# Performance work log

Hardware: AMD Instinct MI355X
Metric: run time of the kernel (lower is better)

Reference implementation:

```python
import jax, jax.numpy as jnp
import numpy as np

BATCH, SEQ, D_IN, D_STATE = 8, 4096, 1024, 64


def setup_inputs() -> dict:
    key = jax.random.key(0)
    ks = jax.random.split(key, 3)
    u = jax.random.normal(ks[0], (BATCH, SEQ, D_IN), dtype=jnp.float32)
    log_A = jnp.zeros((D_STATE,), dtype=jnp.float32)
    B = jax.random.normal(ks[1], (D_STATE, D_IN), dtype=jnp.float32) * 0.01
    C = jax.random.normal(ks[2], (D_IN, D_STATE), dtype=jnp.float32) * 0.01
    D = jnp.ones((D_IN,), dtype=jnp.float32)
    log_delta = jnp.zeros((D_IN,), dtype=jnp.float32)
    return {"u": u, "log_A": log_A, "B": B, "C": C, "D": D, "log_delta": log_delta}


def reference(u, log_A, B, C, D, log_delta):
    batch, seq_len, input_dim = u.shape
    state_dim = log_A.shape[0]
    delta = jax.nn.softplus(log_delta)                      # [I]
    A = -jnp.exp(log_A)                                     # [N]
    A_bar = jnp.exp(delta[:, None] * A[None, :])            # [I, N]
    A_bar_state = A_bar.mean(axis=0)                        # [N]
    B_bar = B * delta[None, :]                              # [N, I]
    # Precompute input projections for all timesteps: [B, T, N]
    Bu = jnp.einsum('ni,bti->btn', B_bar, u)
    x0 = jnp.zeros((batch, state_dim), dtype=u.dtype)

    def step(x, bu_t):
        x = x * A_bar_state[None, :] + bu_t
        return x, x

    _, xs = jax.lax.scan(step, x0, jnp.swapaxes(Bu, 0, 1))  # xs: [T, B, N]
    xs = jnp.swapaxes(xs, 0, 1)                             # [B, T, N]
    y = jnp.einsum('in,btn->bti', C, xs) + D[None, None, :] * u
    return y
```

## Files before the change

kernel.cpp:

```cpp
#include <hip/hip_runtime.h>
#include <hip/hip_bf16.h>
#include <cstdint>

#define BATCH 8
#define SEQ   4096
#define DIN   1024
#define DST   64
#define CHUNK 64
#define NC    (SEQ/CHUNK)

typedef __attribute__((ext_vector_type(8))) short short8;
typedef __attribute__((ext_vector_type(4))) short short4v;
typedef __attribute__((ext_vector_type(4))) float f32x4;

__device__ __forceinline__ short f2bf(float f) {
    union { float f; unsigned u; } v; v.f = f;
    unsigned r = v.u + 0x7fffu + ((v.u >> 16) & 1u);
    return (short)(r >> 16);
}
__device__ __forceinline__ float softplus_f(float x) {
    return (x > 20.f) ? x : log1pf(expf(x));
}

__global__ void ssm_k0(const float* __restrict__ logA, const float* __restrict__ Bm,
                       const float* __restrict__ Cm, const float* __restrict__ logdelta,
                       short* __restrict__ Bb, short* __restrict__ Cb,
                       float* __restrict__ a_o, float* __restrict__ l2a_o,
                       float* __restrict__ aL_o)
{
    __shared__ float red[256];
    int blk = blockIdx.x, tid = threadIdx.x;
    if (blk < DST) {
        int n = blk;
        float An = -expf(logA[n]);
        float acc = 0.f;
        #pragma unroll
        for (int ii = 0; ii < DIN/256; ++ii) {
            int i = ii*256 + tid;
            float dlt = softplus_f(logdelta[i]);
            Bb[n*DIN + i] = f2bf(Bm[n*DIN + i] * dlt);
            acc += expf(dlt * An);
        }
        red[tid] = acc; __syncthreads();
        for (int s = 128; s > 0; s >>= 1) {
            if (tid < s) red[tid] += red[tid + s];
            __syncthreads();
        }
        if (tid == 0) {
            float a = red[0] * (1.f/DIN);
            a_o[n]   = a;
            l2a_o[n] = log2f(a);
            float p = a;
            #pragma unroll
            for (int q = 0; q < 6; ++q) p = p*p;
            aL_o[n] = p;
        }
    } else {
        int base = (blk - DST) * (DIN*DST/16);
        for (int e = tid; e < DIN*DST/16; e += 256)
            Cb[base + e] = f2bf(Cm[base + e]);
    }
}

__global__ __launch_bounds__(512) void ssm_k1(
    const float* __restrict__ u, const short* __restrict__ Bb,
    const float* __restrict__ a_i, float* __restrict__ xloc, float* __restrict__ carry)
{
    int blk = blockIdx.x;
    int b = blk >> 6, c = blk & (NC-1);
    int tid = threadIdx.x;
    int w = tid >> 6, lane = tid & 63;
    int wr = w & 3, wk = w >> 2;
    int m = lane & 15, quad = lane >> 4;

    long row = ((long)b << 12) + (c << 6) + (wr << 4) + m;
    const float* up  = u  + row * DIN + wk*(DIN/2) + quad * 8;
    const short* bb0 = Bb + wk*(DIN/2) + quad * 8;

    f32x4 acc0 = {0,0,0,0}, acc1 = {0,0,0,0}, acc2 = {0,0,0,0}, acc3 = {0,0,0,0};

    #pragma unroll 4
    for (int ks = 0; ks < DIN/64; ++ks) {
        const float4* uv = (const float4*)(up + ks*32);
        float4 ua = uv[0];
        float4 ub = uv[1];
        short8 af;
        af[0]=f2bf(ua.x); af[1]=f2bf(ua.y); af[2]=f2bf(ua.z); af[3]=f2bf(ua.w);
        af[4]=f2bf(ub.x); af[5]=f2bf(ub.y); af[6]=f2bf(ub.z); af[7]=f2bf(ub.w);
        const short* bbase = bb0 + ks*32;
        short8 b0 = *(const short8*)(bbase + ( 0 + m)*DIN);
        short8 b1 = *(const short8*)(bbase + (16 + m)*DIN);
        short8 b2 = *(const short8*)(bbase + (32 + m)*DIN);
        short8 b3 = *(const short8*)(bbase + (48 + m)*DIN);
        acc0 = __builtin_amdgcn_mfma_f32_16x16x32_bf16(af, b0, acc0, 0,0,0);
        acc1 = __builtin_amdgcn_mfma_f32_16x16x32_bf16(af, b1, acc1, 0,0,0);
        acc2 = __builtin_amdgcn_mfma_f32_16x16x32_bf16(af, b2, acc2, 0,0,0);
        acc3 = __builtin_amdgcn_mfma_f32_16x16x32_bf16(af, b3, acc3, 0,0,0);
    }

    __shared__ float bu[2][CHUNK][DST];
    int trow = (wr << 4) + (quad << 2);
    #pragma unroll
    for (int r = 0; r < 4; ++r) {
        bu[wk][trow + r][ 0 + m] = acc0[r];
        bu[wk][trow + r][16 + m] = acc1[r];
        bu[wk][trow + r][32 + m] = acc2[r];
        bu[wk][trow + r][48 + m] = acc3[r];
    }
    __syncthreads();

    if (tid < DST) {
        int n = tid;
        float an = a_i[n];
        float x = 0.f;
        float* xp = xloc + (((long)b << 12) + (c << 6)) * DST + n;
        #pragma unroll 8
        for (int t = 0; t < CHUNK; ++t) {
            x = x * an + (bu[0][t][n] + bu[1][t][n]);
            xp[(long)t * DST] = x;
        }
        carry[(b * NC + c) * DST + n] = x;
    }
}

__global__ void ssm_k2(const float* __restrict__ carry, const float* __restrict__ aL,
                       float* __restrict__ Xin)
{
    int b = blockIdx.x, n = threadIdx.x;
    float cr[NC];
    #pragma unroll
    for (int c = 0; c < NC; ++c)
        cr[c] = carry[(b*NC + c)*DST + n];
    float x = 0.f, al = aL[n];
    #pragma unroll
    for (int c = 0; c < NC; ++c) {
        Xin[(b*NC + c)*DST + n] = x;
        x = x * al + cr[c];
    }
}

__global__ __launch_bounds__(256) void ssm_k3(
    const float* __restrict__ u, const float* __restrict__ xloc,
    const float* __restrict__ Xin, const float* __restrict__ l2a,
    const short* __restrict__ Cb, const float* __restrict__ Dv,
    float* __restrict__ y)
{
    int tblk = blockIdx.x;
    long t0 = (long)tblk << 4;
    int b = (int)(t0 >> 12);
    int tloc0 = (int)(t0 & (SEQ-1));
    int chunk = tloc0 >> 6;
    int jbase = tloc0 & (CHUNK-1);

    __shared__ short xb[16][DST];

    int tid = threadIdx.x;
    {
        int m  = tid >> 4;
        int n0 = (tid & 15) * 4;
        long t = t0 + m;
        int j  = jbase + m;
        float4 xv = *(const float4*)(xloc + t*DST + n0);
        float4 xi = *(const float4*)(Xin + (long)(b*NC + chunk)*DST + n0);
        float4 la = *(const float4*)(l2a + n0);
        float jp = (float)(j + 1);
        short4v xs;
        xs[0] = f2bf(xv.x + exp2f(jp*la.x)*xi.x);
        xs[1] = f2bf(xv.y + exp2f(jp*la.y)*xi.y);
        xs[2] = f2bf(xv.z + exp2f(jp*la.z)*xi.z);
        xs[3] = f2bf(xv.w + exp2f(jp*la.w)*xi.w);
        *(short4v*)(&xb[m][n0]) = xs;
    }
    __syncthreads();

    int w = tid >> 6, lane = tid & 63;
    int l16 = lane & 15, quad = lane >> 4;

    short8 x0 = *(const short8*)(&xb[l16][ 0 + quad*8]);
    short8 x1 = *(const short8*)(&xb[l16][32 + quad*8]);

    long trow = t0 + l16;
    const float* urow = u + trow*DIN;
    float* yrow = y + trow*DIN;

    #pragma unroll 4
    for (int ii = 0; ii < 16; ++ii) {
        int i0 = (ii*4 + w) * 16;
        const short* cb = Cb + (long)(i0 + l16)*DST + quad*8;
        short8 c0 = *(const short8*)(cb);
        short8 c1 = *(const short8*)(cb + 32);
        f32x4 acc = {0,0,0,0};
        acc = __builtin_amdgcn_mfma_f32_16x16x32_bf16(c0, x0, acc, 0,0,0);
        acc = __builtin_amdgcn_mfma_f32_16x16x32_bf16(c1, x1, acc, 0,0,0);
        int ib = i0 + (quad << 2);
        float4 dd = *(const float4*)(Dv + ib);
        float4 uu = *(const float4*)(urow + ib);
        float4 o;
        o.x = acc[0] + dd.x*uu.x;
        o.y = acc[1] + dd.y*uu.y;
        o.z = acc[2] + dd.z*uu.z;
        o.w = acc[3] + dd.w*uu.w;
        *(float4*)(yrow + ib) = o;
    }
}

extern "C" void kernel_launch(void* const* d_in, const int* in_sizes, int n_in,
                              void* d_out, int out_size, void* d_ws, size_t ws_size,
                              hipStream_t stream)
{
    const float* u        = (const float*)d_in[0];
    const float* logA     = (const float*)d_in[1];
    const float* Bm       = (const float*)d_in[2];
    const float* Cm       = (const float*)d_in[3];
    const float* D        = (const float*)d_in[4];
    const float* logdelta = (const float*)d_in[5];
    float* y = (float*)d_out;

    char* ws = (char*)d_ws;
    float* xloc  = (float*)(ws);
    float* carry = (float*)(ws + 8u*1024*1024);
    float* Xin   = (float*)(ws + 8u*1024*1024 + 128*1024);
    short* Bb    = (short*)(ws + 8u*1024*1024 + 256*1024);
    short* Cb    = (short*)(ws + 8u*1024*1024 + 384*1024);
    float* a_o   = (float*)(ws + 8u*1024*1024 + 512*1024);
    float* l2a_o = a_o + 64;
    float* aL_o  = a_o + 128;

    hipLaunchKernelGGL(ssm_k0, dim3(DST + 16), dim3(256), 0, stream,
                       logA, Bm, Cm, logdelta, Bb, Cb, a_o, l2a_o, aL_o);
    hipLaunchKernelGGL(ssm_k1, dim3(BATCH*NC), dim3(512), 0, stream,
                       u, Bb, a_o, xloc, carry);
    hipLaunchKernelGGL(ssm_k2, dim3(BATCH), dim3(DST), 0, stream,
                       carry, aL_o, Xin);
    hipLaunchKernelGGL(ssm_k3, dim3((BATCH*SEQ)/16), dim3(256), 0, stream,
                       u, xloc, Xin, l2a_o, Cb, D, y);
}
```

Before: 320.0 us.

## Fuse chunk scan, carry propagation and output projection into one kernel with decoupled lookback

Merges the per-chunk Bu GEMM and local scan, the cross-chunk carry scan, and the C projection plus D*u into a single kernel. Chunks are ordered by an atomic ticket, and each chunk gets its carry-in through a decoupled lookback over global flags. The local states stay in LDS, so the 8MB xloc buffer is never written and read back, and two kernel launches go away. The cost is serialized lookback spin waits, a second pass over u inside the same block, and only 512 blocks doing the output GEMM instead of 2048.

Measured after the change: 405.6 us. 26.7% more time.

```diff
diff --git a/kernel.cpp b/kernel.cpp
--- a/kernel.cpp
+++ b/kernel.cpp
@@ -1,5 +1,4 @@
 #include <hip/hip_runtime.h>
-#include <hip/hip_bf16.h>
 #include <cstdint>
 
 #define BATCH 8
@@ -8,9 +7,9 @@
 #define DST   64
 #define CHUNK 64
 #define NC    (SEQ/CHUNK)
+#define NBLK  (BATCH*NC)
 
 typedef __attribute__((ext_vector_type(8))) short short8;
-typedef __attribute__((ext_vector_type(4))) short short4v;
 typedef __attribute__((ext_vector_type(4))) float f32x4;
 
 __device__ __forceinline__ short f2bf(float f) {
@@ -26,7 +25,7 @@
                        const float* __restrict__ Cm, const float* __restrict__ logdelta,
                        short* __restrict__ Bb, short* __restrict__ Cb,
                        float* __restrict__ a_o, float* __restrict__ l2a_o,
-                       float* __restrict__ aL_o)
+                       float* __restrict__ aL_o, unsigned* __restrict__ ctl)
 {
     __shared__ float red[256];
     int blk = blockIdx.x, tid = threadIdx.x;
@@ -56,151 +55,156 @@
             aL_o[n] = p;
         }
     } else {
+        if (blk == DST) {
+            for (int g = tid; g <= NBLK; g += 256) ctl[g] = 0u;
+        }
         int base = (blk - DST) * (DIN*DST/16);
         for (int e = tid; e < DIN*DST/16; e += 256)
             Cb[base + e] = f2bf(Cm[base + e]);
     }
 }
 
-__global__ __launch_bounds__(512) void ssm_k1(
+__global__ __launch_bounds__(512, 4) void ssm_fused(
     const float* __restrict__ u, const short* __restrict__ Bb,
-    const float* __restrict__ a_i, float* __restrict__ xloc, float* __restrict__ carry)
+    const short* __restrict__ Cb, const float* __restrict__ a_i,
+    const float* __restrict__ l2a, const float* __restrict__ aLp,
+    const float* __restrict__ Dv, unsigned* __restrict__ ctl,
+    float* __restrict__ carryG, float* __restrict__ inclG,
+    float* __restrict__ y)
 {
-    int blk = blockIdx.x;
-    int b = blk >> 6, c = blk & (NC-1);
+    __shared__ float bu[2][CHUNK][DST];
+    __shared__ short xs[CHUNK][DST];
+    __shared__ float E_lds[DST];
+    __shared__ unsigned vb_sh;
+
     int tid = threadIdx.x;
+    if (tid == 0) vb_sh = atomicAdd(&ctl[NBLK], 1u);
+    __syncthreads();
+    int vb = (int)vb_sh;
+    int b = vb >> 6, c = vb & (NC-1);
+
     int w = tid >> 6, lane = tid & 63;
-    int wr = w & 3, wk = w >> 2;
     int m = lane & 15, quad = lane >> 4;
 
-    long row = ((long)b << 12) + (c << 6) + (wr << 4) + m;
-    const float* up  = u  + row * DIN + wk*(DIN/2) + quad * 8;
-    const short* bb0 = Bb + wk*(DIN/2) + quad * 8;
-
-    f32x4 acc0 = {0,0,0,0}, acc1 = {0,0,0,0}, acc2 = {0,0,0,0}, acc3 = {0,0,0,0};
-
-    #pragma unroll 4
-    for (int ks = 0; ks < DIN/64; ++ks) {
-        const float4* uv = (const float4*)(up + ks*32);
-        float4 ua = uv[0];
-        float4 ub = uv[1];
-        short8 af;
-        af[0]=f2bf(ua.x); af[1]=f2bf(ua.y); af[2]=f2bf(ua.z); af[3]=f2bf(ua.w);
-        af[4]=f2bf(ub.x); af[5]=f2bf(ub.y); af[6]=f2bf(ub.z); af[7]=f2bf(ub.w);
-        const short* bbase = bb0 + ks*32;
-        short8 b0 = *(const short8*)(bbase + ( 0 + m)*DIN);
-        short8 b1 = *(const short8*)(bbase + (16 + m)*DIN);
-        short8 b2 = *(const short8*)(bbase + (32 + m)*DIN);
-        short8 b3 = *(const short8*)(bbase + (48 + m)*DIN);
-        acc0 = __builtin_amdgcn_mfma_f32_16x16x32_bf16(af, b0, acc0, 0,0,0);
-        acc1 = __builtin_amdgcn_mfma_f32_16x16x32_bf16(af, b1, acc1, 0,0,0);
-        acc2 = __builtin_amdgcn_mfma_f32_16x16x32_bf16(af, b2, acc2, 0,0,0);
-        acc3 = __builtin_amdgcn_mfma_f32_16x16x32_bf16(af, b3, acc3, 0,0,0);
-    }
-
-    __shared__ float bu[2][CHUNK][DST];
-    int trow = (wr << 4) + (quad << 2);
-    #pragma unroll
-    for (int r = 0; r < 4; ++r) {
-        bu[wk][trow + r][ 0 + m] = acc0[r];
-        bu[wk][trow + r][16 + m] = acc1[r];
-        bu[wk][trow + r][32 + m] = acc2[r];
-        bu[wk][trow + r][48 + m] = acc3[r];
+    {
+        int wr = w & 3, wk = w >> 2;
+        long row = ((long)b << 12) + (c << 6) + (wr << 4) + m;
+        const float* up  = u  + row * DIN + wk*(DIN/2) + quad*8;
+        const short* bb0 = Bb + wk*(DIN/2) + quad*8;
+        f32x4 acc0={0,0,0,0}, acc1={0,0,0,0}, acc2={0,0,0,0}, acc3={0,0,0,0};
+        #pragma unroll 4
+        for (int ks = 0; ks < DIN/64; ++ks) {
+            const float4* uv = (const float4*)(up + ks*32);
+            float4 ua = uv[0], ub2 = uv[1];
+            short8 af;
+            af[0]=f2bf(ua.x);  af[1]=f2bf(ua.y);  af[2]=f2bf(ua.z);  af[3]=f2bf(ua.w);
+            af[4]=f2bf(ub2.x); af[5]=f2bf(ub2.y); af[6]=f2bf(ub2.z); af[7]=f2bf(ub2.w);
+            const short* bbase = bb0 + ks*32;
+            short8 b0 = *(const short8*)(bbase + ( 0 + m)*DIN);
+            short8 b1 = *(const short8*)(bbase + (16 + m)*DIN);
+            short8 b2 = *(const short8*)(bbase + (32 + m)*DIN);
+            short8 b3 = *(const short8*)(bbase + (48 + m)*DIN);
+            acc0 = __builtin_amdgcn_mfma_f32_16x16x32_bf16(af, b0, acc0, 0,0,0);
+            acc1 = __builtin_amdgcn_mfma_f32_16x16x32_bf16(af, b1, acc1, 0,0,0);
+            acc2 = __builtin_amdgcn_mfma_f32_16x16x32_bf16(af, b2, acc2, 0,0,0);
+            acc3 = __builtin_amdgcn_mfma_f32_16x16x32_bf16(af, b3, acc3, 0,0,0);
+        }
+        int trow = (wr << 4) + (quad << 2);
+        #pragma unroll
+        for (int r = 0; r < 4; ++r) {
+            bu[wk][trow + r][ 0 + m] = acc0[r];
+            bu[wk][trow + r][16 + m] = acc1[r];
+            bu[wk][trow + r][32 + m] = acc2[r];
+            bu[wk][trow + r][48 + m] = acc3[r];
+        }
     }
     __syncthreads();
 
     if (tid < DST) {
         int n = tid;
-        float an = a_i[n];
+        float an  = a_i[n];
+        float aLn = aLp[n];
         float x = 0.f;
-        float* xp = xloc + (((long)b << 12) + (c << 6)) * DST + n;
         #pragma unroll 8
         for (int t = 0; t < CHUNK; ++t) {
             x = x * an + (bu[0][t][n] + bu[1][t][n]);
-            xp[(long)t * DST] = x;
-        }
-        carry[(b * NC + c) * DST + n] = x;
-    }
-}
-
-__global__ void ssm_k2(const float* __restrict__ carry, const float* __restrict__ aL,
-                       float* __restrict__ Xin)
-{
-    int b = blockIdx.x, n = threadIdx.x;
-    float cr[NC];
-    #pragma unroll
-    for (int c = 0; c < NC; ++c)
-        cr[c] = carry[(b*NC + c)*DST + n];
-    float x = 0.f, al = aL[n];
-    #pragma unroll
-    for (int c = 0; c < NC; ++c) {
-        Xin[(b*NC + c)*DST + n] = x;
-        x = x * al + cr[c];
-    }
-}
-
-__global__ __launch_bounds__(256) void ssm_k3(
-    const float* __restrict__ u, const float* __restrict__ xloc,
-    const float* __restrict__ Xin, const float* __restrict__ l2a,
-    const short* __restrict__ Cb, const float* __restrict__ Dv,
-    float* __restrict__ y)
-{
-    int tblk = blockIdx.x;
-    long t0 = (long)tblk << 4;
-    int b = (int)(t0 >> 12);
-    int tloc0 = (int)(t0 & (SEQ-1));
-    int chunk = tloc0 >> 6;
-    int jbase = tloc0 & (CHUNK-1);
-
-    __shared__ short xb[16][DST];
-
-    int tid = threadIdx.x;
+            bu[0][t][n] = x;
+        }
+        float E = 0.f;
+        if (c > 0) {
+            __hip_atomic_store(&carryG[vb*DST + n], x, __ATOMIC_RELAXED, __HIP_MEMORY_SCOPE_AGENT);
+            if (n == 0)
+                __hip_atomic_store(&ctl[vb], 1u, __ATOMIC_RELEASE, __HIP_MEMORY_SCOPE_AGENT);
+            float f = 1.f;
+            for (int p = vb - 1; ; --p) {
+                unsigned st = 0;
+                if (n == 0) {
+                    st = __hip_atomic_load(&ctl[p], __ATOMIC_ACQUIRE, __HIP_MEMORY_SCOPE_AGENT);
+                    while (st == 0u) {
+                        __builtin_amdgcn_s_sleep(2);
+                        st = __hip_atomic_load(&ctl[p], __ATOMIC_ACQUIRE, __HIP_MEMORY_SCOPE_AGENT);
+                    }
+                }
+                st = (unsigned)__shfl((int)st, 0);
+                if (st == 2u) {
+                    E += f * __hip_atomic_load(&inclG[p*DST + n], __ATOMIC_RELAXED, __HIP_MEMORY_SCOPE_AGENT);
+                    break;
+                }
+                E += f * __hip_atomic_load(&carryG[p*DST + n], __ATOMIC_RELAXED, __HIP_MEMORY_SCOPE_AGENT);
+                f *= aLn;
+            }
+        }
+        __hip_atomic_store(&inclG[vb*DST + n], x + aLn * E, __ATOMIC_RELAXED, __HIP_MEMORY_SCOPE_AGENT);
+        if (n == 0)
+            __hip_atomic_store(&ctl[vb], 2u, __ATOMIC_RELEASE, __HIP_MEMORY_SCOPE_AGENT);
+        E_lds[n] = E;
+    }
+    __syncthreads();
+
     {
-        int m  = tid >> 4;
-        int n0 = (tid & 15) * 4;
-        long t = t0 + m;
-        int j  = jbase + m;
-        float4 xv = *(const float4*)(xloc + t*DST + n0);
-        float4 xi = *(const float4*)(Xin + (long)(b*NC + chunk)*DST + n0);
-        float4 la = *(const float4*)(l2a + n0);
-        float jp = (float)(j + 1);
-        short4v xs;
-        xs[0] = f2bf(xv.x + exp2f(jp*la.x)*xi.x);
-        xs[1] = f2bf(xv.y + exp2f(jp*la.y)*xi.y);
-        xs[2] = f2bf(xv.z + exp2f(jp*la.z)*xi.z);
-        xs[3] = f2bf(xv.w + exp2f(jp*la.w)*xi.w);
-        *(short4v*)(&xb[m][n0]) = xs;
-    }
-    __syncthreads();
-
-    int w = tid >> 6, lane = tid & 63;
-    int l16 = lane & 15, quad = lane >> 4;
-
-    short8 x0 = *(const short8*)(&xb[l16][ 0 + quad*8]);
-    short8 x1 = *(const short8*)(&xb[l16][32 + quad*8]);
-
-    long trow = t0 + l16;
-    const float* urow = u + trow*DIN;
-    float* yrow = y + trow*DIN;
-
-    #pragma unroll 4
-    for (int ii = 0; ii < 16; ++ii) {
-        int i0 = (ii*4 + w) * 16;
-        const short* cb = Cb + (long)(i0 + l16)*DST + quad*8;
-        short8 c0 = *(const short8*)(cb);
-        short8 c1 = *(const short8*)(cb + 32);
-        f32x4 acc = {0,0,0,0};
-        acc = __builtin_amdgcn_mfma_f32_16x16x32_bf16(c0, x0, acc, 0,0,0);
-        acc = __builtin_amdgcn_mfma_f32_16x16x32_bf16(c1, x1, acc, 0,0,0);
-        int ib = i0 + (quad << 2);
-        float4 dd = *(const float4*)(Dv + ib);
-        float4 uu = *(const float4*)(urow + ib);
-        float4 o;
-        o.x = acc[0] + dd.x*uu.x;
-        o.y = acc[1] + dd.y*uu.y;
-        o.z = acc[2] + dd.z*uu.z;
-        o.w = acc[3] + dd.w*uu.w;
-        *(float4*)(yrow + ib) = o;
+        int t  = tid >> 3;
+        int n0 = (tid & 7) * 8;
+        float jp = (float)(t + 1);
+        float xv[8];
+        #pragma unroll
+        for (int k2 = 0; k2 < 8; ++k2) {
+            int n = n0 + k2;
+            xv[k2] = bu[0][t][n] + exp2f(jp * l2a[n]) * E_lds[n];
+        }
+        short8 xsv;
+        #pragma unroll
+        for (int k2 = 0; k2 < 8; ++k2) xsv[k2] = f2bf(xv[k2]);
+        *(short8*)(&xs[t][n0]) = xsv;
+    }
+    __syncthreads();
+
+    {
+        int l16 = lane & 15;
+        int tt = w & 3, ihalf = w >> 2;
+        short8 x0 = *(const short8*)(&xs[tt*16 + l16][ 0 + quad*8]);
+        short8 x1 = *(const short8*)(&xs[tt*16 + l16][32 + quad*8]);
+        long trow = ((long)b << 12) + (c << 6) + tt*16 + l16;
+        const float* urow = u + trow * DIN;
+        float* yrow = y + trow * DIN;
+        #pragma unroll 4
+        for (int ii = 0; ii < 32; ++ii) {
+            int i0 = (ihalf*32 + ii) * 16;
+            const short* cb = Cb + (long)(i0 + l16)*DST + quad*8;
+            short8 c0 = *(const short8*)(cb);
+            short8 c1 = *(const short8*)(cb + 32);
+            f32x4 acc = {0,0,0,0};
+            acc = __builtin_amdgcn_mfma_f32_16x16x32_bf16(c0, x0, acc, 0,0,0);
+            acc = __builtin_amdgcn_mfma_f32_16x16x32_bf16(c1, x1, acc, 0,0,0);
+            int ib = i0 + (quad << 2);
+            float4 dd = *(const float4*)(Dv + ib);
+            float4 uu = *(const float4*)(urow + ib);
+            float4 o;
+            o.x = acc[0] + dd.x*uu.x;
+            o.y = acc[1] + dd.y*uu.y;
+            o.z = acc[2] + dd.z*uu.z;
+            o.w = acc[3] + dd.w*uu.w;
+            *(float4*)(yrow + ib) = o;
+        }
     }
 }
 
@@ -217,21 +221,17 @@
     float* y = (float*)d_out;
 
     char* ws = (char*)d_ws;
-    float* xloc  = (float*)(ws);
-    float* carry = (float*)(ws + 8u*1024*1024);
-    float* Xin   = (float*)(ws + 8u*1024*1024 + 128*1024);
-    short* Bb    = (short*)(ws + 8u*1024*1024 + 256*1024);
-    short* Cb    = (short*)(ws + 8u*1024*1024 + 384*1024);
-    float* a_o   = (float*)(ws + 8u*1024*1024 + 512*1024);
-    float* l2a_o = a_o + 64;
-    float* aL_o  = a_o + 128;
+    unsigned* ctl   = (unsigned*)(ws);
+    float*    carry = (float*)(ws + 4*1024);
+    float*    incl  = (float*)(ws + 4*1024 + 128*1024);
+    short*    Bb    = (short*)(ws + 4*1024 + 256*1024);
+    short*    Cb    = (short*)(ws + 4*1024 + 384*1024);
+    float*    a_o   = (float*)(ws + 4*1024 + 512*1024);
+    float*    l2a_o = a_o + 64;
+    float*    aL_o  = a_o + 128;
 
     hipLaunchKernelGGL(ssm_k0, dim3(DST + 16), dim3(256), 0, stream,
-                       logA, Bm, Cm, logdelta, Bb, Cb, a_o, l2a_o, aL_o);
-    hipLaunchKernelGGL(ssm_k1, dim3(BATCH*NC), dim3(512), 0, stream,
-                       u, Bb, a_o, xloc, carry);
-    hipLaunchKernelGGL(ssm_k2, dim3(BATCH), dim3(DST), 0, stream,
-                       carry, aL_o, Xin);
-    hipLaunchKernelGGL(ssm_k3, dim3((BATCH*SEQ)/16), dim3(256), 0, stream,
-                       u, xloc, Xin, l2a_o, Cb, D, y);
-}
+                       logA, Bm, Cm, logdelta, Bb, Cb, a_o, l2a_o, aL_o, ctl);
+    hipLaunchKernelGGL(ssm_fused, dim3(NBLK), dim3(512), 0, stream,
+                       u, Bb, Cb, a_o, l2a_o, aL_o, D, ctl, carry, incl, y);
+}
```

## Halve scan chunk size and fold carry propagation into output kernel

Applied to the files above, without the earlier changes.

Shrinks the chunk size from 64 to 32, so the projection kernel launches twice as many 256-thread blocks. This fills more compute units and shortens each block's serial intra-chunk scan. The separate inter-chunk carry kernel, a serial 8-block launch, is removed. Each output block now recomputes its incoming state from all preceding chunk carries, which adds redundant serial work of up to 127 steps per block in exchange for one fewer launch and less serial time on the critical path. LDS arrays are also padded to reduce bank conflicts.

After: 318.2 us. Within noise of the previous version (-0.6%).

```diff
diff --git a/kernel.cpp b/kernel.cpp
--- a/kernel.cpp
+++ b/kernel.cpp
@@ -1,13 +1,13 @@
 #include <hip/hip_runtime.h>
-#include <hip/hip_bf16.h>
 #include <cstdint>
 
 #define BATCH 8
 #define SEQ   4096
 #define DIN   1024
 #define DST   64
-#define CHUNK 64
-#define NC    (SEQ/CHUNK)
+#define CHUNK 32
+#define NCC   (SEQ/CHUNK)
+#define NBLK1 (BATCH*NCC)
 
 typedef __attribute__((ext_vector_type(8))) short short8;
 typedef __attribute__((ext_vector_type(4))) short short4v;
@@ -52,7 +52,7 @@
             l2a_o[n] = log2f(a);
             float p = a;
             #pragma unroll
-            for (int q = 0; q < 6; ++q) p = p*p;
+            for (int q = 0; q < 5; ++q) p = p*p;
             aL_o[n] = p;
         }
     } else {
@@ -62,18 +62,18 @@
     }
 }
 
-__global__ __launch_bounds__(512) void ssm_k1(
+__global__ __launch_bounds__(256) void ssm_k1(
     const float* __restrict__ u, const short* __restrict__ Bb,
     const float* __restrict__ a_i, float* __restrict__ xloc, float* __restrict__ carry)
 {
     int blk = blockIdx.x;
-    int b = blk >> 6, c = blk & (NC-1);
+    int b = blk >> 7, cc = blk & (NCC-1);
     int tid = threadIdx.x;
     int w = tid >> 6, lane = tid & 63;
-    int wr = w & 3, wk = w >> 2;
+    int wr = w & 1, wk = w >> 1;
     int m = lane & 15, quad = lane >> 4;
 
-    long row = ((long)b << 12) + (c << 6) + (wr << 4) + m;
+    long row = ((long)b << 12) + (cc << 5) + (wr << 4) + m;
     const float* up  = u  + row * DIN + wk*(DIN/2) + quad * 8;
     const short* bb0 = Bb + wk*(DIN/2) + quad * 8;
 
@@ -98,7 +98,7 @@
         acc3 = __builtin_amdgcn_mfma_f32_16x16x32_bf16(af, b3, acc3, 0,0,0);
     }
 
-    __shared__ float bu[2][CHUNK][DST];
+    __shared__ float bu[2][CHUNK][DST+1];
     int trow = (wr << 4) + (quad << 2);
     #pragma unroll
     for (int r = 0; r < 4; ++r) {
@@ -113,71 +113,68 @@
         int n = tid;
         float an = a_i[n];
         float x = 0.f;
-        float* xp = xloc + (((long)b << 12) + (c << 6)) * DST + n;
-        #pragma unroll 8
+        float* xp = xloc + (((long)b << 12) + (cc << 5)) * DST + n;
+        #pragma unroll
         for (int t = 0; t < CHUNK; ++t) {
             x = x * an + (bu[0][t][n] + bu[1][t][n]);
             xp[(long)t * DST] = x;
         }
-        carry[(b * NC + c) * DST + n] = x;
-    }
-}
-
-__global__ void ssm_k2(const float* __restrict__ carry, const float* __restrict__ aL,
-                       float* __restrict__ Xin)
-{
-    int b = blockIdx.x, n = threadIdx.x;
-    float cr[NC];
-    #pragma unroll
-    for (int c = 0; c < NC; ++c)
-        cr[c] = carry[(b*NC + c)*DST + n];
-    float x = 0.f, al = aL[n];
-    #pragma unroll
-    for (int c = 0; c < NC; ++c) {
-        Xin[(b*NC + c)*DST + n] = x;
-        x = x * al + cr[c];
+        carry[blk * DST + n] = x;
     }
 }
 
 __global__ __launch_bounds__(256) void ssm_k3(
     const float* __restrict__ u, const float* __restrict__ xloc,
-    const float* __restrict__ Xin, const float* __restrict__ l2a,
-    const short* __restrict__ Cb, const float* __restrict__ Dv,
-    float* __restrict__ y)
+    const float* __restrict__ carry, const float* __restrict__ aLp,
+    const float* __restrict__ l2a, const short* __restrict__ Cb,
+    const float* __restrict__ Dv, float* __restrict__ y)
 {
     int tblk = blockIdx.x;
     long t0 = (long)tblk << 4;
     int b = (int)(t0 >> 12);
     int tloc0 = (int)(t0 & (SEQ-1));
-    int chunk = tloc0 >> 6;
+    int c = tloc0 >> 5;
     int jbase = tloc0 & (CHUNK-1);
 
-    __shared__ short xb[16][DST];
+    __shared__ float E_lds[DST];
+    __shared__ short xs[16][72];
 
     int tid = threadIdx.x;
+    if (tid < DST) {
+        int n = tid;
+        float al = aLp[n];
+        float E = 0.f;
+        const float* cp = carry + (b*NCC)*DST + n;
+        #pragma unroll 4
+        for (int p = 0; p < c; ++p)
+            E = E * al + cp[p*DST];
+        E_lds[n] = E;
+    }
+    __syncthreads();
+
     {
         int m  = tid >> 4;
         int n0 = (tid & 15) * 4;
         long t = t0 + m;
         int j  = jbase + m;
         float4 xv = *(const float4*)(xloc + t*DST + n0);
-        float4 xi = *(const float4*)(Xin + (long)(b*NC + chunk)*DST + n0);
         float4 la = *(const float4*)(l2a + n0);
+        float4 Ev = *(const float4*)(&E_lds[n0]);
         float jp = (float)(j + 1);
-        short4v xs;
-        xs[0] = f2bf(xv.x + exp2f(jp*la.x)*xi.x);
-        xs[1] = f2bf(xv.y + exp2f(jp*la.y)*xi.y);
-        xs[2] = f2bf(xv.z + exp2f(jp*la.z)*xi.z);
-        xs[3] = f2bf(xv.w + exp2f(jp*la.w)*xi.w);
-        *(short4v*)(&xb[m][n0]) = xs;
+        short4v xsv;
+        xsv[0] = f2bf(xv.x + exp2f(jp*la.x)*Ev.x);
+        xsv[1] = f2bf(xv.y + exp2f(jp*la.y)*Ev.y);
+        xsv[2] = f2bf(xv.z + exp2f(jp*la.z)*Ev.z);
+        xsv[3] = f2bf(xv.w + exp2f(jp*la.w)*Ev.w);
+        *(short4v*)(&xs[m][n0]) = xsv;
     }
     __syncthreads();
 
     int w = tid >> 6, lane = tid & 63;
     int l16 = lane & 15, quad = lane >> 4;
 
-    short8 x0 = *(const short8*)(&xb[l16][ 0 + quad*8]);
-    short8 x1 = *(const short8*)(&xb[l16][32 + quad*8]);
+    short8 x0 = *(const short8*)(&xs[l16][ 0 + quad*8]);
+    short8 x1 = *(const short8*)(&xs[l16][32 + quad*8]);
 
     long trow = t0 + l16;
     const float* urow = u + trow*DIN;
@@ -219,7 +216,6 @@
     char* ws = (char*)d_ws;
     float* xloc  = (float*)(ws);
     float* carry = (float*)(ws + 8u*1024*1024);
-    float* Xin   = (float*)(ws + 8u*1024*1024 + 128*1024);
     short* Bb    = (short*)(ws + 8u*1024*1024 + 256*1024);
     short* Cb    = (short*)(ws + 8u*1024*1024 + 384*1024);
     float* a_o   = (float*)(ws + 8u*1024*1024 + 512*1024);
@@ -228,10 +224,8 @@
 
     hipLaunchKernelGGL(ssm_k0, dim3(DST + 16), dim3(256), 0, stream,
                        logA, Bm, Cm, logdelta, Bb, Cb, a_o, l2a_o, aL_o);
-    hipLaunchKernelGGL(ssm_k1, dim3(BATCH*NC), dim3(512), 0, stream,
+    hipLaunchKernelGGL(ssm_k1, dim3(NBLK1), dim3(256), 0, stream,
                        u, Bb, a_o, xloc, carry);
-    hipLaunchKernelGGL(ssm_k2, dim3(BATCH), dim3(DST), 0, stream,
-                       carry, aL_o, Xin);
     hipLaunchKernelGGL(ssm_k3, dim3((BATCH*SEQ)/16), dim3(256), 0, stream,
-                       u, xloc, Xin, l2a_o, Cb, D, y);
-}
+                       u, xloc, carry, aL_o, l2a_o, Cb, D, y);
+}
```
